# Performance work log

Hardware: AMD Instinct MI355X
Metric: run time of the kernel (lower is better)

The kernel has to match this reference:

```python
import jax, jax.numpy as jnp
import numpy as np

EPS = 1e-8  # torch.nn.CosineSimilarity default eps


def setup_inputs() -> dict:
    key = jax.random.key(0)
    batch = jax.random.normal(key, (8192, 128), dtype=jnp.float32)
    return {"batch": batch}


def reference(batch):
    B = batch.shape[0]
    # Full pairwise cosine similarity matrix S[i, j]
    norms = jnp.linalg.norm(batch, axis=1)                      # [B]
    denom = jnp.maximum(norms[:, None] * norms[None, :], EPS)   # [B, B]
    S = (batch @ batch.T) / denom                                # [B, B]
    # Denominator of soft_nll(i, j): sum_{m != i} exp(S[i, m])
    expS = jnp.exp(S)
    Z = expS.sum(axis=1) - jnp.diagonal(expS)                    # [B]
    logZ = jnp.log(Z)                                            # [B]
    # term(i, j) = -log( exp(S[i,j]) / Z_i ) = -S[i,j] + logZ_i
    # Original loop: for k in 1..(B+1)//2 - 1, pairs (2k-1, 2k) 1-indexed
    N = (B + 1) // 2
    ks = jnp.arange(1, N)
    i = 2 * ks - 2  # 0-indexed first element of pair
    j = 2 * ks - 1  # 0-indexed second element of pair
    pair_loss = (-S[i, j] + logZ[i]) + (-S[j, i] + logZ[j])
    return jnp.sum(pair_loss) / B
```

## Files before the change

### kernel.cpp

```cpp
#include <hip/hip_runtime.h>
#include <hip/hip_bf16.h>

typedef __attribute__((ext_vector_type(8))) short short8;
typedef __attribute__((ext_vector_type(4))) float floatx4;

#define B_ROWS 8192
#define DIM 128
#define NPAIR 4095
#define RSCALE 1.2011224087864498f

#define GLOAD_LDS16(gp, lp)                                                     \
    __builtin_amdgcn_global_load_lds(                                           \
        (const __attribute__((address_space(1))) void*)(gp),                    \
        (__attribute__((address_space(3))) void*)(lp), 16, 0, 0)

__global__ void kzero(float* __restrict__ Z) {
    int i = blockIdx.x * 256 + threadIdx.x;
    if (i < B_ROWS) Z[i] = 0.f;
}

__global__ void kprep(const float* __restrict__ X, __hip_bfloat16* __restrict__ XN,
                      float* __restrict__ pairT, float* __restrict__ out) {
    __shared__ float2 lds[4][64];
    const int wid = threadIdx.x >> 6;
    const int lane = threadIdx.x & 63;
    const int row = blockIdx.x * 4 + wid;

    const float2 v = *reinterpret_cast<const float2*>(X + row * DIM + lane * 2);
    float ss = v.x * v.x + v.y * v.y;
    #pragma unroll
    for (int m = 1; m < 64; m <<= 1) ss += __shfl_xor(ss, m, 64);
    const float rn = ss > 0.f ? rsqrtf(ss) : 0.f;
    const float2 nv = make_float2(v.x * rn, v.y * rn);

    *reinterpret_cast<__hip_bfloat162*>(XN + row * DIM + lane * 2) =
        __float22bfloat162_rn(make_float2(nv.x * RSCALE, nv.y * RSCALE));
    lds[wid][lane] = nv;
    __syncthreads();

    if ((wid & 1) == 0) {
        const int p = blockIdx.x * 2 + (wid >> 1);
        if (p < NPAIR) {
            const float2 a = lds[wid][lane];
            const float2 b = lds[wid + 1][lane];
            float d = a.x * b.x + a.y * b.y;
            #pragma unroll
            for (int m = 1; m < 64; m <<= 1) d += __shfl_xor(d, m, 64);
            if (lane == 0) pairT[p] = d;
        }
    }
    if (blockIdx.x == 0 && threadIdx.x == 0) out[0] = 0.f;
}

__device__ __forceinline__ void stage_half(const __hip_bfloat16* __restrict__ gsrc,
                                           __hip_bfloat16* lbuf, int tid) {
    const int wid = tid >> 6;
    const int lane = tid & 63;
    #pragma unroll
    for (int it = 0; it < 4; ++it) {
        const int woff = it * 2048 + wid * 512;
        const int e = woff + lane * 8;
        const int src = (e & ~127) | ((e & 127) ^ (((e >> 7) & 7) << 3));
        GLOAD_LDS16(gsrc + src, lbuf + woff);
    }
}

template <bool USEP>
__global__ void __launch_bounds__(256, 2) kgemm(const __hip_bfloat16* __restrict__ XN,
                                                float* __restrict__ ZP) {
    __shared__ __hip_bfloat16 Bs[3][64 * DIM];

    const int tid = threadIdx.x;
    const int wid = tid >> 6;
    const int lane = tid & 63;
    const int lr = lane & 15;
    const int lk = lane >> 4;
    const int wr = wid >> 1;
    const int wc = wid & 1;
    const int rb = blockIdx.y;
    const int g = blockIdx.x;

    short8 a[4][4];
    const __hip_bfloat16* Abase = XN + (rb * 128 + wr * 64 + lr) * DIM + lk * 8;
    #pragma unroll
    for (int m = 0; m < 4; ++m)
        #pragma unroll
        for (int kk = 0; kk < 4; ++kk)
            a[kk][m] = *reinterpret_cast<const short8*>(Abase + m * 16 * DIM + kk * 32);

    float rp[4][4];
    #pragma unroll
    for (int m = 0; m < 4; ++m)
        #pragma unroll
        for (int r = 0; r < 4; ++r) rp[m][r] = 0.f;

    const floatx4 zero4 = {0.f, 0.f, 0.f, 0.f};

    stage_half(XN + (size_t)(g * 8) * 128 * DIM, Bs[0], tid);
    stage_half(XN + ((size_t)(g * 8) * 128 + 64) * DIM, Bs[1], tid);

    for (int t = 0; t < 16; ++t) {
        if (t < 15)
            asm volatile("s_waitcnt vmcnt(4)" ::: "memory");
        else
            asm volatile("s_waitcnt vmcnt(0)" ::: "memory");
        __builtin_amdgcn_s_barrier();

        if (t + 2 < 16)
            stage_half(XN + ((size_t)(g * 8 + ((t + 2) >> 1)) * 128 + ((t + 2) & 1) * 64) * DIM,
                       Bs[(t + 2) % 3], tid);

        const __hip_bfloat16* Bt = Bs[t % 3];
        const int cbj = g * 8 + (t >> 1);
        const bool dzero = (cbj == rb) && ((t & 1) == wr);

        __builtin_amdgcn_s_setprio(1);
        short8 b[4][2];
        #pragma unroll
        for (int n = 0; n < 2; ++n) {
            const int row = wc * 32 + n * 16 + lr;
            #pragma unroll
            for (int kk = 0; kk < 4; ++kk) {
                const int col = (kk * 32 + lk * 8) ^ ((row & 7) << 3);
                b[kk][n] = *reinterpret_cast<const short8*>(&Bt[row * DIM + col]);
            }
        }

        floatx4 acc[4][2];
        #pragma unroll
        for (int m = 0; m < 4; ++m)
            #pragma unroll
            for (int n = 0; n < 2; ++n)
                acc[m][n] = __builtin_amdgcn_mfma_f32_16x16x32_bf16(a[0][m], b[0][n], zero4, 0, 0, 0);
        #pragma unroll
        for (int kk = 1; kk < 4; ++kk)
            #pragma unroll
            for (int m = 0; m < 4; ++m)
                #pragma unroll
                for (int n = 0; n < 2; ++n)
                    acc[m][n] = __builtin_amdgcn_mfma_f32_16x16x32_bf16(a[kk][m], b[kk][n], acc[m][n], 0, 0, 0);
        __builtin_amdgcn_s_setprio(0);

        if (dzero) {
            #pragma unroll
            for (int m = 0; m < 4; ++m)
                #pragma unroll
                for (int n = 0; n < 2; ++n)
                    #pragma unroll
                    for (int r = 0; r < 4; ++r) {
                        float e = __builtin_amdgcn_exp2f(acc[m][n][r]);
                        if (m * 16 + lk * 4 + r == wc * 32 + n * 16 + lr) e = 0.f;
                        rp[m][r] += e;
                    }
        } else {
            #pragma unroll
            for (int m = 0; m < 4; ++m)
                #pragma unroll
                for (int n = 0; n < 2; ++n)
                    #pragma unroll
                    for (int r = 0; r < 4; ++r)
                        rp[m][r] += __builtin_amdgcn_exp2f(acc[m][n][r]);
        }
    }

    #pragma unroll
    for (int m = 0; m < 4; ++m)
        #pragma unroll
        for (int r = 0; r < 4; ++r) {
            float v = rp[m][r];
            v += __shfl_xor(v, 1, 64);
            v += __shfl_xor(v, 2, 64);
            v += __shfl_xor(v, 4, 64);
            v += __shfl_xor(v, 8, 64);
            if (lr == 0) {
                const int row = rb * 128 + wr * 64 + m * 16 + lk * 4 + r;
                if (USEP)
                    ZP[(g * 2 + wc) * B_ROWS + row] = v;
                else
                    atomicAdd(&ZP[row], v);
            }
        }
}

__global__ void kfinalP(const float* __restrict__ P, const float* __restrict__ pairT,
                        float* __restrict__ out) {
    const int r = blockIdx.x * 256 + threadIdx.x;
    float s = 0.f;
    if (r < B_ROWS - 2) {
        float z = 0.f;
        #pragma unroll
        for (int tt = 0; tt < 16; ++tt) z += P[tt * B_ROWS + r];
        s = logf(z);
    }
    if (r < NPAIR) s -= 2.f * pairT[r];
    #pragma unroll
    for (int m = 1; m < 64; m <<= 1) s += __shfl_xor(s, m, 64);
    __shared__ float red[4];
    const int wid = threadIdx.x >> 6;
    const int lane = threadIdx.x & 63;
    if (lane == 0) red[wid] = s;
    __syncthreads();
    if (threadIdx.x == 0) {
        float tsum = red[0] + red[1] + red[2] + red[3];
        atomicAdd(out, tsum / (float)B_ROWS);
    }
}

__global__ void kfinalZ(const float* __restrict__ Z, const float* __restrict__ pairT,
                        float* __restrict__ out) {
    float s = 0.f;
    for (int r = threadIdx.x; r < B_ROWS - 2; r += 1024) s += logf(Z[r]);
    for (int p = threadIdx.x; p < NPAIR; p += 1024) s -= 2.f * pairT[p];
    #pragma unroll
    for (int m = 1; m < 64; m <<= 1) s += __shfl_xor(s, m, 64);
    __shared__ float red[16];
    const int wid = threadIdx.x >> 6;
    const int lane = threadIdx.x & 63;
    if (lane == 0) red[wid] = s;
    __syncthreads();
    if (threadIdx.x == 0) {
        float t = 0.f;
        #pragma unroll
        for (int i = 0; i < 16; ++i) t += red[i];
        out[0] = t / (float)B_ROWS;
    }
}

extern "C" void kernel_launch(void* const* d_in, const int* in_sizes, int n_in,
                              void* d_out, int out_size, void* d_ws, size_t ws_size,
                              hipStream_t stream) {
    (void)in_sizes; (void)n_in; (void)out_size;
    const float* X = (const float*)d_in[0];
    float* out = (float*)d_out;
    char* ws = (char*)d_ws;

    float* Z = (float*)ws;
    float* pairT = (float*)(ws + 32768);
    __hip_bfloat16* XN = (__hip_bfloat16*)(ws + 49152);
    float* P = (float*)(ws + 49152 + 2097152);
    const size_t need = 49152 + 2097152 + (size_t)16 * B_ROWS * 4;
    const bool useP = ws_size >= need;

    kprep<<<2048, 256, 0, stream>>>(X, XN, pairT, out);
    if (useP) {
        kgemm<true><<<dim3(8, 64), 256, 0, stream>>>(XN, P);
        kfinalP<<<32, 256, 0, stream>>>(P, pairT, out);
    } else {
        kzero<<<32, 256, 0, stream>>>(Z);
        kgemm<false><<<dim3(8, 64), 256, 0, stream>>>(XN, Z);
        kfinalZ<<<1, 1024, 0, stream>>>(Z, pairT, out);
    }
}
```

Measured before the change: 34.05 us.

## Exploit symmetry of the similarity matrix to halve GEMM and exp work

Each block now processes only block-diagonal offsets 0..32 of the 64x64 tile grid, scheduled as d = g + 11*i over an 11-wide grid. For off-diagonal tiles it accumulates exp row sums and also exp column sums, since exp(S) is symmetric. This roughly halves the MFMA and exp work. The cost is extra cross-lane shuffles and column-partial writes, and kfinalP must reduce 84 partial slots instead of 16, which raises workspace size and final-pass memory traffic.

```diff
diff --git a/kernel.cpp b/kernel.cpp
--- a/kernel.cpp
+++ b/kernel.cpp
@@ -7,6 +7,7 @@
 #define B_ROWS 8192
 #define DIM 128
 #define NPAIR 4095
+#define NSLOT 84
 #define RSCALE 1.2011224087864498f
 
 #define GLOAD_LDS16(gp, lp)                                                     \
@@ -96,23 +97,32 @@
 
     const floatx4 zero4 = {0.f, 0.f, 0.f, 0.f};
 
-    stage_half(XN + (size_t)(g * 8) * 128 * DIM, Bs[0], tid);
-    stage_half(XN + ((size_t)(g * 8) * 128 + 64) * DIM, Bs[1], tid);
-
-    for (int t = 0; t < 16; ++t) {
-        if (t < 15)
+    {
+        const size_t base = (size_t)(((rb + g) & 63) * 128) * DIM;
+        stage_half(XN + base, Bs[0], tid);
+        stage_half(XN + base + 64 * DIM, Bs[1], tid);
+    }
+
+    #pragma unroll
+    for (int s = 0; s < 6; ++s) {
+        if (s < 5)
             asm volatile("s_waitcnt vmcnt(4)" ::: "memory");
         else
             asm volatile("s_waitcnt vmcnt(0)" ::: "memory");
         __builtin_amdgcn_s_barrier();
 
-        if (t + 2 < 16)
-            stage_half(XN + ((size_t)(g * 8 + ((t + 2) >> 1)) * 128 + ((t + 2) & 1) * 64) * DIM,
-                       Bs[(t + 2) % 3], tid);
-
-        const __hip_bfloat16* Bt = Bs[t % 3];
-        const int cbj = g * 8 + (t >> 1);
-        const bool dzero = (cbj == rb) && ((t & 1) == wr);
+        if (s + 2 < 6) {
+            const int ii = (s + 2) >> 1, hh = (s + 2) & 1;
+            const int ccb = (rb + g + 11 * ii) & 63;
+            stage_half(XN + ((size_t)(ccb * 128) + hh * 64) * DIM, Bs[(s + 2) % 3], tid);
+        }
+
+        const int i = s >> 1, half = s & 1;
+        const int d = g + 11 * i;
+        const int cb = (rb + d) & 63;
+        const bool dzero = (d == 0) && (half == wr);
+        const bool docol = (d >= 1) && (d <= 31);
+        const __hip_bfloat16* Bt = Bs[s % 3];
 
         __builtin_amdgcn_s_setprio(1);
         short8 b[4][2];
@@ -141,25 +151,33 @@
                     acc[m][n] = __builtin_amdgcn_mfma_f32_16x16x32_bf16(a[kk][m], b[kk][n], acc[m][n], 0, 0, 0);
         __builtin_amdgcn_s_setprio(0);
 
-        if (dzero) {
-            #pragma unroll
-            for (int m = 0; m < 4; ++m)
+        float cp[2] = {0.f, 0.f};
+        #pragma unroll
+        for (int m = 0; m < 4; ++m)
+            #pragma unroll
+            for (int n = 0; n < 2; ++n)
                 #pragma unroll
-                for (int n = 0; n < 2; ++n)
-                    #pragma unroll
-                    for (int r = 0; r < 4; ++r) {
-                        float e = __builtin_amdgcn_exp2f(acc[m][n][r]);
-                        if (m * 16 + lk * 4 + r == wc * 32 + n * 16 + lr) e = 0.f;
-                        rp[m][r] += e;
-                    }
-        } else {
-            #pragma unroll
-            for (int m = 0; m < 4; ++m)
-                #pragma unroll
-                for (int n = 0; n < 2; ++n)
-                    #pragma unroll
-                    for (int r = 0; r < 4; ++r)
-                        rp[m][r] += __builtin_amdgcn_exp2f(acc[m][n][r]);
+                for (int r = 0; r < 4; ++r) {
+                    float e = __builtin_amdgcn_exp2f(acc[m][n][r]);
+                    if (dzero && (m * 16 + lk * 4 + r == wc * 32 + n * 16 + lr)) e = 0.f;
+                    rp[m][r] += e;
+                    cp[n] += e;
+                }
+
+        if (docol) {
+            #pragma unroll
+            for (int n = 0; n < 2; ++n) {
+                float v = cp[n];
+                v += __shfl_xor(v, 16, 64);
+                v += __shfl_xor(v, 32, 64);
+                if (lane < 16) {
+                    const int col = cb * 128 + half * 64 + wc * 32 + n * 16 + lr;
+                    if (USEP)
+                        ZP[(22 + (d - 1) * 2 + wr) * B_ROWS + col] = v;
+                    else
+                        atomicAdd(&ZP[col], v);
+                }
+            }
         }
     }
 
@@ -188,8 +206,7 @@
     float s = 0.f;
     if (r < B_ROWS - 2) {
         float z = 0.f;
-        #pragma unroll
-        for (int tt = 0; tt < 16; ++tt) z += P[tt * B_ROWS + r];
+        for (int tt = 0; tt < NSLOT; ++tt) z += P[tt * B_ROWS + r];
         s = logf(z);
     }
     if (r < NPAIR) s -= 2.f * pairT[r];
@@ -238,16 +255,16 @@
     float* pairT = (float*)(ws + 32768);
     __hip_bfloat16* XN = (__hip_bfloat16*)(ws + 49152);
     float* P = (float*)(ws + 49152 + 2097152);
-    const size_t need = 49152 + 2097152 + (size_t)16 * B_ROWS * 4;
+    const size_t need = 49152 + 2097152 + (size_t)NSLOT * B_ROWS * 4;
     const bool useP = ws_size >= need;
 
     kprep<<<2048, 256, 0, stream>>>(X, XN, pairT, out);
     if (useP) {
-        kgemm<true><<<dim3(8, 64), 256, 0, stream>>>(XN, P);
+        kgemm<true><<<dim3(11, 64), 256, 0, stream>>>(XN, P);
         kfinalP<<<32, 256, 0, stream>>>(P, pairT, out);
     } else {
         kzero<<<32, 256, 0, stream>>>(Z);
-        kgemm<false><<<dim3(8, 64), 256, 0, stream>>>(XN, Z);
+        kgemm<false><<<dim3(11, 64), 256, 0, stream>>>(XN, Z);
         kfinalZ<<<1, 1024, 0, stream>>>(Z, pairT, out);
     }
 }
```

Result: slower. 39.93 us (+17.3%).

## Fuse prep, GEMM and final reduction into one cooperative kernel with grid syncs

Applied to the files above, without the earlier changes.

Replaces the three-kernel chain (normalize, GEMM+exp row sums, final log reduction) with a single cooperative kernel that uses grid-wide syncs between phases. The aim is to remove launch gaps and inter-kernel overhead. The pair dot products are now read from the GEMM accumulators on diagonal tiles instead of being computed in the prep phase. This relies on all 512 blocks being co-resident, and the grid syncs add their own cost. If the cooperative launch fails, it falls back to the old path.

```diff
diff --git a/kernel.cpp b/kernel.cpp
--- a/kernel.cpp
+++ b/kernel.cpp
@@ -1,5 +1,8 @@
 #include <hip/hip_runtime.h>
 #include <hip/hip_bf16.h>
+#include <hip/hip_cooperative_groups.h>
+
+namespace cg = cooperative_groups;
 
 typedef __attribute__((ext_vector_type(8))) short short8;
 typedef __attribute__((ext_vector_type(4))) float floatx4;
@@ -8,15 +11,191 @@
 #define DIM 128
 #define NPAIR 4095
 #define RSCALE 1.2011224087864498f
+#define LN2F 0.6931471805599453f
 
 #define GLOAD_LDS16(gp, lp)                                                     \
     __builtin_amdgcn_global_load_lds(                                           \
         (const __attribute__((address_space(1))) void*)(gp),                    \
         (__attribute__((address_space(3))) void*)(lp), 16, 0, 0)
 
-__global__ void kzero(float* __restrict__ Z) {
-    int i = blockIdx.x * 256 + threadIdx.x;
-    if (i < B_ROWS) Z[i] = 0.f;
+__device__ __forceinline__ void stage_half(const __hip_bfloat16* __restrict__ gsrc,
+                                           __hip_bfloat16* lbuf, int tid) {
+    const int wid = tid >> 6;
+    const int lane = tid & 63;
+    #pragma unroll
+    for (int it = 0; it < 4; ++it) {
+        const int woff = it * 2048 + wid * 512;
+        const int e = woff + lane * 8;
+        const int src = (e & ~127) | ((e & 127) ^ (((e >> 7) & 7) << 3));
+        GLOAD_LDS16(gsrc + src, lbuf + woff);
+    }
+}
+
+__global__ void __launch_bounds__(256, 2) kfused(const float* __restrict__ X,
+                                                 __hip_bfloat16* __restrict__ XN,
+                                                 float* __restrict__ P,
+                                                 float* __restrict__ pairT,
+                                                 float* __restrict__ out) {
+    __shared__ __hip_bfloat16 Bs[3][64 * DIM];
+
+    const int tid = threadIdx.x;
+    const int wid = tid >> 6;
+    const int lane = tid & 63;
+    const int lr = lane & 15;
+    const int lk = lane >> 4;
+    const int wr = wid >> 1;
+    const int wc = wid & 1;
+    const int g = blockIdx.x;
+    const int rb = blockIdx.y;
+    const int bidl = rb * 8 + g;
+
+    #pragma unroll
+    for (int rr = 0; rr < 4; ++rr) {
+        const int row = bidl * 16 + wid * 4 + rr;
+        const float2 v = *reinterpret_cast<const float2*>(X + row * DIM + lane * 2);
+        float ss = v.x * v.x + v.y * v.y;
+        #pragma unroll
+        for (int m = 1; m < 64; m <<= 1) ss += __shfl_xor(ss, m, 64);
+        const float rn = (ss > 0.f ? rsqrtf(ss) : 0.f) * RSCALE;
+        *reinterpret_cast<__hip_bfloat162*>(XN + row * DIM + lane * 2) =
+            __float22bfloat162_rn(make_float2(v.x * rn, v.y * rn));
+    }
+    if (bidl == 0 && tid == 0) out[0] = 0.f;
+
+    cg::this_grid().sync();
+
+    {
+        short8 a[4][4];
+        const __hip_bfloat16* Abase = XN + (rb * 128 + wr * 64 + lr) * DIM + lk * 8;
+        #pragma unroll
+        for (int m = 0; m < 4; ++m)
+            #pragma unroll
+            for (int kk = 0; kk < 4; ++kk)
+                a[kk][m] = *reinterpret_cast<const short8*>(Abase + m * 16 * DIM + kk * 32);
+
+        float rp[4][4];
+        #pragma unroll
+        for (int m = 0; m < 4; ++m)
+            #pragma unroll
+            for (int r = 0; r < 4; ++r) rp[m][r] = 0.f;
+
+        const floatx4 zero4 = {0.f, 0.f, 0.f, 0.f};
+
+        stage_half(XN + (size_t)(g * 8) * 128 * DIM, Bs[0], tid);
+        stage_half(XN + ((size_t)(g * 8) * 128 + 64) * DIM, Bs[1], tid);
+
+        for (int t = 0; t < 16; ++t) {
+            if (t < 15)
+                asm volatile("s_waitcnt vmcnt(4)" ::: "memory");
+            else
+                asm volatile("s_waitcnt vmcnt(0)" ::: "memory");
+            __builtin_amdgcn_s_barrier();
+
+            if (t + 2 < 16)
+                stage_half(XN + ((size_t)(g * 8 + ((t + 2) >> 1)) * 128 + ((t + 2) & 1) * 64) * DIM,
+                           Bs[(t + 2) % 3], tid);
+
+            const __hip_bfloat16* Bt = Bs[t % 3];
+            const int cbj = g * 8 + (t >> 1);
+            const bool dzero = (cbj == rb) && ((t & 1) == wr);
+
+            __builtin_amdgcn_s_setprio(1);
+            short8 b[4][2];
+            #pragma unroll
+            for (int n = 0; n < 2; ++n) {
+                const int row = wc * 32 + n * 16 + lr;
+                #pragma unroll
+                for (int kk = 0; kk < 4; ++kk) {
+                    const int col = (kk * 32 + lk * 8) ^ ((row & 7) << 3);
+                    b[kk][n] = *reinterpret_cast<const short8*>(&Bt[row * DIM + col]);
+                }
+            }
+
+            floatx4 acc[4][2];
+            #pragma unroll
+            for (int m = 0; m < 4; ++m)
+                #pragma unroll
+                for (int n = 0; n < 2; ++n)
+                    acc[m][n] = __builtin_amdgcn_mfma_f32_16x16x32_bf16(a[0][m], b[0][n], zero4, 0, 0, 0);
+            #pragma unroll
+            for (int kk = 1; kk < 4; ++kk)
+                #pragma unroll
+                for (int m = 0; m < 4; ++m)
+                    #pragma unroll
+                    for (int n = 0; n < 2; ++n)
+                        acc[m][n] = __builtin_amdgcn_mfma_f32_16x16x32_bf16(a[kk][m], b[kk][n], acc[m][n], 0, 0, 0);
+            __builtin_amdgcn_s_setprio(0);
+
+            if (dzero) {
+                #pragma unroll
+                for (int m = 0; m < 4; ++m)
+                    #pragma unroll
+                    for (int n = 0; n < 2; ++n)
+                        #pragma unroll
+                        for (int r = 0; r < 4; ++r) {
+                            const int Rl = m * 16 + lk * 4 + r;
+                            const int Cl = wc * 32 + n * 16 + lr;
+                            const float av = acc[m][n][r];
+                            float e = __builtin_amdgcn_exp2f(av);
+                            if (Rl == Cl) e = 0.f;
+                            rp[m][r] += e;
+                            if (Cl == Rl + 1 && (Rl & 1) == 0) {
+                                const int Rg = rb * 128 + wr * 64 + Rl;
+                                if (Rg < B_ROWS - 2) pairT[Rg >> 1] = av * LN2F;
+                            }
+                        }
+            } else {
+                #pragma unroll
+                for (int m = 0; m < 4; ++m)
+                    #pragma unroll
+                    for (int n = 0; n < 2; ++n)
+                        #pragma unroll
+                        for (int r = 0; r < 4; ++r)
+                            rp[m][r] += __builtin_amdgcn_exp2f(acc[m][n][r]);
+            }
+        }
+
+        #pragma unroll
+        for (int m = 0; m < 4; ++m)
+            #pragma unroll
+            for (int r = 0; r < 4; ++r) {
+                float v = rp[m][r];
+                v += __shfl_xor(v, 1, 64);
+                v += __shfl_xor(v, 2, 64);
+                v += __shfl_xor(v, 4, 64);
+                v += __shfl_xor(v, 8, 64);
+                if (lr == 0) {
+                    const int row = rb * 128 + wr * 64 + m * 16 + lk * 4 + r;
+                    P[(g * 2 + wc) * B_ROWS + row] = v;
+                }
+            }
+    }
+
+    cg::this_grid().sync();
+
+    {
+        float s = 0.f;
+        if (tid < 16) {
+            const int r = bidl * 16 + tid;
+            if (r < B_ROWS - 2) {
+                float z = 0.f;
+                #pragma unroll
+                for (int t = 0; t < 16; ++t) z += P[t * B_ROWS + r];
+                s = logf(z);
+            }
+        } else if (tid < 24) {
+            const int p = bidl * 8 + (tid - 16);
+            if (p < NPAIR) s = -2.f * pairT[p];
+        }
+        #pragma unroll
+        for (int m = 1; m < 64; m <<= 1) s += __shfl_xor(s, m, 64);
+        float* red = (float*)&Bs[0][0];
+        __syncthreads();
+        if (lane == 0) red[wid] = s;
+        __syncthreads();
+        if (tid == 0)
+            atomicAdd(out, (red[0] + red[1] + red[2] + red[3]) / (float)B_ROWS);
+    }
 }
 
 __global__ void kprep(const float* __restrict__ X, __hip_bfloat16* __restrict__ XN,
@@ -52,20 +231,6 @@
     if (blockIdx.x == 0 && threadIdx.x == 0) out[0] = 0.f;
 }
 
-__device__ __forceinline__ void stage_half(const __hip_bfloat16* __restrict__ gsrc,
-                                           __hip_bfloat16* lbuf, int tid) {
-    const int wid = tid >> 6;
-    const int lane = tid & 63;
-    #pragma unroll
-    for (int it = 0; it < 4; ++it) {
-        const int woff = it * 2048 + wid * 512;
-        const int e = woff + lane * 8;
-        const int src = (e & ~127) | ((e & 127) ^ (((e >> 7) & 7) << 3));
-        GLOAD_LDS16(gsrc + src, lbuf + woff);
-    }
-}
-
-template <bool USEP>
 __global__ void __launch_bounds__(256, 2) kgemm(const __hip_bfloat16* __restrict__ XN,
                                                 float* __restrict__ ZP) {
     __shared__ __hip_bfloat16 Bs[3][64 * DIM];
@@ -174,10 +339,8 @@
             v += __shfl_xor(v, 8, 64);
             if (lr == 0) {
                 const int row = rb * 128 + wr * 64 + m * 16 + lk * 4 + r;
-                if (USEP)
-                    ZP[(g * 2 + wc) * B_ROWS + row] = v;
-                else
-                    atomicAdd(&ZP[row], v);
+                P_STORE:
+                ZP[(g * 2 + wc) * B_ROWS + row] = v;
             }
         }
 }
@@ -206,48 +369,24 @@
     }
 }
 
-__global__ void kfinalZ(const float* __restrict__ Z, const float* __restrict__ pairT,
-                        float* __restrict__ out) {
-    float s = 0.f;
-    for (int r = threadIdx.x; r < B_ROWS - 2; r += 1024) s += logf(Z[r]);
-    for (int p = threadIdx.x; p < NPAIR; p += 1024) s -= 2.f * pairT[p];
-    #pragma unroll
-    for (int m = 1; m < 64; m <<= 1) s += __shfl_xor(s, m, 64);
-    __shared__ float red[16];
-    const int wid = threadIdx.x >> 6;
-    const int lane = threadIdx.x & 63;
-    if (lane == 0) red[wid] = s;
-    __syncthreads();
-    if (threadIdx.x == 0) {
-        float t = 0.f;
-        #pragma unroll
-        for (int i = 0; i < 16; ++i) t += red[i];
-        out[0] = t / (float)B_ROWS;
-    }
-}
-
 extern "C" void kernel_launch(void* const* d_in, const int* in_sizes, int n_in,
                               void* d_out, int out_size, void* d_ws, size_t ws_size,
                               hipStream_t stream) {
-    (void)in_sizes; (void)n_in; (void)out_size;
+    (void)in_sizes; (void)n_in; (void)out_size; (void)ws_size;
     const float* X = (const float*)d_in[0];
     float* out = (float*)d_out;
     char* ws = (char*)d_ws;
 
-    float* Z = (float*)ws;
-    float* pairT = (float*)(ws + 32768);
-    __hip_bfloat16* XN = (__hip_bfloat16*)(ws + 49152);
-    float* P = (float*)(ws + 49152 + 2097152);
-    const size_t need = 49152 + 2097152 + (size_t)16 * B_ROWS * 4;
-    const bool useP = ws_size >= need;
-
-    kprep<<<2048, 256, 0, stream>>>(X, XN, pairT, out);
-    if (useP) {
-        kgemm<true><<<dim3(8, 64), 256, 0, stream>>>(XN, P);
+    float* pairT = (float*)ws;
+    __hip_bfloat16* XN = (__hip_bfloat16*)(ws + 32768);
+    float* P = (float*)(ws + 32768 + 2097152);
+
+    void* args[] = {(void*)&X, (void*)&XN, (void*)&P, (void*)&pairT, (void*)&out};
+    hipError_t e = hipLaunchCooperativeKernel((const void*)kfused, dim3(8, 64),
+                                              dim3(256), args, 0, stream);
+    if (e != hipSuccess) {
+        kprep<<<2048, 256, 0, stream>>>(X, XN, pairT, out);
+        kgemm<<<dim3(8, 64), 256, 0, stream>>>(XN, P);
         kfinalP<<<32, 256, 0, stream>>>(P, pairT, out);
-    } else {
-        kzero<<<32, 256, 0, stream>>>(Z);
-        kgemm<false><<<dim3(8, 64), 256, 0, stream>>>(XN, Z);
-        kfinalZ<<<1, 1024, 0, stream>>>(Z, pairT, out);
-    }
-}
+    }
+}
```

Measured after the change: 135.5 us. 3.98x slower.

## Switch Gram matrix to FP8 scaled MFMA 32x32x64 with doubled column split

Applied to the files above, without the earlier changes.

Normalized rows are now stored as FP8 (e4m3) instead of bf16, and the similarity GEMM uses the 32x32x64 scaled f8f6f4 MFMA. This halves the bytes for the operand and LDS tiles and doubles the math rate per instruction. The grid is split into 16 column groups (32 partial slots), so each block processes 8 tiles instead of 16. kprep now handles two rows per wave and computes the pair dot products with shuffles instead of LDS. FP8 quantization of the normalized vectors adds error in S and in the exponentiated sums, which may hurt the accuracy tolerance.

```diff
diff --git a/kernel.cpp b/kernel.cpp
--- a/kernel.cpp
+++ b/kernel.cpp
@@ -1,12 +1,14 @@
 #include <hip/hip_runtime.h>
 #include <hip/hip_bf16.h>
 
-typedef __attribute__((ext_vector_type(8))) short short8;
-typedef __attribute__((ext_vector_type(4))) float floatx4;
+typedef __attribute__((ext_vector_type(4))) int intx4;
+typedef __attribute__((ext_vector_type(8))) int intx8;
+typedef __attribute__((ext_vector_type(16))) float floatx16;
 
 #define B_ROWS 8192
 #define DIM 128
 #define NPAIR 4095
+#define NSLOT 32
 #define RSCALE 1.2011224087864498f
 
 #define GLOAD_LDS16(gp, lp)                                                     \
@@ -19,161 +21,159 @@
     if (i < B_ROWS) Z[i] = 0.f;
 }
 
-__global__ void kprep(const float* __restrict__ X, __hip_bfloat16* __restrict__ XN,
+__global__ void kprep(const float* __restrict__ X, unsigned char* __restrict__ XN,
                       float* __restrict__ pairT, float* __restrict__ out) {
-    __shared__ float2 lds[4][64];
     const int wid = threadIdx.x >> 6;
     const int lane = threadIdx.x & 63;
-    const int row = blockIdx.x * 4 + wid;
-
-    const float2 v = *reinterpret_cast<const float2*>(X + row * DIM + lane * 2);
-    float ss = v.x * v.x + v.y * v.y;
-    #pragma unroll
-    for (int m = 1; m < 64; m <<= 1) ss += __shfl_xor(ss, m, 64);
+    const int j = lane & 31;
+    const int W = blockIdx.x * 4 + wid;
+    const int row = 2 * W + (lane >> 5);
+
+    const float4 v = *reinterpret_cast<const float4*>(X + row * DIM + j * 4);
+    float ss = v.x * v.x + v.y * v.y + v.z * v.z + v.w * v.w;
+    #pragma unroll
+    for (int m = 1; m < 32; m <<= 1) ss += __shfl_xor(ss, m, 64);
     const float rn = ss > 0.f ? rsqrtf(ss) : 0.f;
-    const float2 nv = make_float2(v.x * rn, v.y * rn);
-
-    *reinterpret_cast<__hip_bfloat162*>(XN + row * DIM + lane * 2) =
-        __float22bfloat162_rn(make_float2(nv.x * RSCALE, nv.y * RSCALE));
-    lds[wid][lane] = nv;
-    __syncthreads();
-
-    if ((wid & 1) == 0) {
-        const int p = blockIdx.x * 2 + (wid >> 1);
-        if (p < NPAIR) {
-            const float2 a = lds[wid][lane];
-            const float2 b = lds[wid + 1][lane];
-            float d = a.x * b.x + a.y * b.y;
-            #pragma unroll
-            for (int m = 1; m < 64; m <<= 1) d += __shfl_xor(d, m, 64);
-            if (lane == 0) pairT[p] = d;
-        }
-    }
-    if (blockIdx.x == 0 && threadIdx.x == 0) out[0] = 0.f;
-}
-
-__device__ __forceinline__ void stage_half(const __hip_bfloat16* __restrict__ gsrc,
-                                           __hip_bfloat16* lbuf, int tid) {
-    const int wid = tid >> 6;
-    const int lane = tid & 63;
-    #pragma unroll
-    for (int it = 0; it < 4; ++it) {
-        const int woff = it * 2048 + wid * 512;
-        const int e = woff + lane * 8;
-        const int src = (e & ~127) | ((e & 127) ^ (((e >> 7) & 7) << 3));
-        GLOAD_LDS16(gsrc + src, lbuf + woff);
+
+    float4 pv;
+    pv.x = __shfl_xor(v.x, 32, 64);
+    pv.y = __shfl_xor(v.y, 32, 64);
+    pv.z = __shfl_xor(v.z, 32, 64);
+    pv.w = __shfl_xor(v.w, 32, 64);
+    float pd = v.x * pv.x + v.y * pv.y + v.z * pv.z + v.w * pv.w;
+    #pragma unroll
+    for (int m = 1; m < 32; m <<= 1) pd += __shfl_xor(pd, m, 64);
+    const float rno = __shfl_xor(rn, 32, 64);
+    if (lane == 0 && W < NPAIR) pairT[W] = pd * rn * rno;
+
+    const float sc = rn * RSCALE;
+    int pk = __builtin_amdgcn_cvt_pk_fp8_f32(v.x * sc, v.y * sc, 0, false);
+    pk = __builtin_amdgcn_cvt_pk_fp8_f32(v.z * sc, v.w * sc, pk, true);
+    reinterpret_cast<int*>(XN)[row * 32 + j] = pk;
+
+    if (W == 0 && lane == 0) out[0] = 0.f;
+}
+
+__device__ __forceinline__ void stage64(const unsigned char* __restrict__ gsrc,
+                                        unsigned char* lbuf, int tid) {
+    #pragma unroll
+    for (int it = 0; it < 2; ++it) {
+        const int off = it * 4096 + tid * 16;
+        const int src = (off & ~127) | ((off & 127) ^ (((off >> 7) & 7) << 4));
+        GLOAD_LDS16(gsrc + src, lbuf + off);
     }
 }
 
 template <bool USEP>
-__global__ void __launch_bounds__(256, 2) kgemm(const __hip_bfloat16* __restrict__ XN,
+__global__ void __launch_bounds__(256, 2) kgemm(const unsigned char* __restrict__ XN,
                                                 float* __restrict__ ZP) {
-    __shared__ __hip_bfloat16 Bs[3][64 * DIM];
+    __shared__ unsigned char Bs[3][64 * DIM];
 
     const int tid = threadIdx.x;
     const int wid = tid >> 6;
     const int lane = tid & 63;
-    const int lr = lane & 15;
-    const int lk = lane >> 4;
+    const int l31 = lane & 31;
+    const int hi = lane >> 5;
     const int wr = wid >> 1;
     const int wc = wid & 1;
     const int rb = blockIdx.y;
     const int g = blockIdx.x;
 
-    short8 a[4][4];
-    const __hip_bfloat16* Abase = XN + (rb * 128 + wr * 64 + lr) * DIM + lk * 8;
-    #pragma unroll
-    for (int m = 0; m < 4; ++m)
-        #pragma unroll
-        for (int kk = 0; kk < 4; ++kk)
-            a[kk][m] = *reinterpret_cast<const short8*>(Abase + m * 16 * DIM + kk * 32);
-
-    float rp[4][4];
-    #pragma unroll
-    for (int m = 0; m < 4; ++m)
-        #pragma unroll
-        for (int r = 0; r < 4; ++r) rp[m][r] = 0.f;
-
-    const floatx4 zero4 = {0.f, 0.f, 0.f, 0.f};
-
-    stage_half(XN + (size_t)(g * 8) * 128 * DIM, Bs[0], tid);
-    stage_half(XN + ((size_t)(g * 8) * 128 + 64) * DIM, Bs[1], tid);
-
-    for (int t = 0; t < 16; ++t) {
-        if (t < 15)
-            asm volatile("s_waitcnt vmcnt(4)" ::: "memory");
+    intx8 a[2][2];
+    #pragma unroll
+    for (int t = 0; t < 2; ++t) {
+        const unsigned char* Ab =
+            XN + (size_t)(rb * 128 + wr * 64 + t * 32 + l31) * DIM + hi * 32;
+        #pragma unroll
+        for (int kk = 0; kk < 2; ++kk)
+            a[kk][t] = *reinterpret_cast<const intx8*>(Ab + kk * 64);
+    }
+
+    float rp[2][16];
+    #pragma unroll
+    for (int t = 0; t < 2; ++t)
+        #pragma unroll
+        for (int q = 0; q < 16; ++q) rp[t][q] = 0.f;
+
+    const floatx16 z16 = {0.f, 0.f, 0.f, 0.f, 0.f, 0.f, 0.f, 0.f,
+                          0.f, 0.f, 0.f, 0.f, 0.f, 0.f, 0.f, 0.f};
+
+    stage64(XN + (size_t)(g * 512) * DIM, Bs[0], tid);
+    stage64(XN + (size_t)(g * 512 + 64) * DIM, Bs[1], tid);
+
+    const int rblk = (rb * 128 + wr * 64) >> 6;
+
+    for (int t = 0; t < 8; ++t) {
+        if (t < 7)
+            asm volatile("s_waitcnt vmcnt(2)" ::: "memory");
         else
             asm volatile("s_waitcnt vmcnt(0)" ::: "memory");
         __builtin_amdgcn_s_barrier();
 
-        if (t + 2 < 16)
-            stage_half(XN + ((size_t)(g * 8 + ((t + 2) >> 1)) * 128 + ((t + 2) & 1) * 64) * DIM,
-                       Bs[(t + 2) % 3], tid);
-
-        const __hip_bfloat16* Bt = Bs[t % 3];
-        const int cbj = g * 8 + (t >> 1);
-        const bool dzero = (cbj == rb) && ((t & 1) == wr);
+        if (t + 2 < 8)
+            stage64(XN + (size_t)(g * 512 + (t + 2) * 64) * DIM, Bs[(t + 2) % 3], tid);
+
+        const unsigned char* Bt = Bs[t % 3];
+        const int cbase = g * 512 + t * 64;
+        const int lcol = wc * 32 + l31;
 
         __builtin_amdgcn_s_setprio(1);
-        short8 b[4][2];
-        #pragma unroll
-        for (int n = 0; n < 2; ++n) {
-            const int row = wc * 32 + n * 16 + lr;
+        intx8 b[2];
+        #pragma unroll
+        for (int kk = 0; kk < 2; ++kk) {
+            const int base = kk * 64 + hi * 32;
+            const int sw = (lcol & 7) << 4;
+            const intx4 lo =
+                *reinterpret_cast<const intx4*>(&Bt[lcol * 128 + (base ^ sw)]);
+            const intx4 hi4 =
+                *reinterpret_cast<const intx4*>(&Bt[lcol * 128 + ((base + 16) ^ sw)]);
+            b[kk] = __builtin_shufflevector(lo, hi4, 0, 1, 2, 3, 4, 5, 6, 7);
+        }
+
+        floatx16 acc[2];
+        #pragma unroll
+        for (int tt = 0; tt < 2; ++tt) {
+            acc[tt] = __builtin_amdgcn_mfma_scale_f32_32x32x64_f8f6f4(
+                a[0][tt], b[0], z16, 0, 0, 0, 0x7F, 0, 0x7F);
+            acc[tt] = __builtin_amdgcn_mfma_scale_f32_32x32x64_f8f6f4(
+                a[1][tt], b[1], acc[tt], 0, 0, 0, 0x7F, 0, 0x7F);
+        }
+        __builtin_amdgcn_s_setprio(0);
+
+        if ((cbase >> 6) == rblk) {
+            const int ccol = cbase + wc * 32 + l31;
             #pragma unroll
-            for (int kk = 0; kk < 4; ++kk) {
-                const int col = (kk * 32 + lk * 8) ^ ((row & 7) << 3);
-                b[kk][n] = *reinterpret_cast<const short8*>(&Bt[row * DIM + col]);
-            }
-        }
-
-        floatx4 acc[4][2];
-        #pragma unroll
-        for (int m = 0; m < 4; ++m)
-            #pragma unroll
-            for (int n = 0; n < 2; ++n)
-                acc[m][n] = __builtin_amdgcn_mfma_f32_16x16x32_bf16(a[0][m], b[0][n], zero4, 0, 0, 0);
-        #pragma unroll
-        for (int kk = 1; kk < 4; ++kk)
-            #pragma unroll
-            for (int m = 0; m < 4; ++m)
+            for (int tt = 0; tt < 2; ++tt)
                 #pragma unroll
-                for (int n = 0; n < 2; ++n)
-                    acc[m][n] = __builtin_amdgcn_mfma_f32_16x16x32_bf16(a[kk][m], b[kk][n], acc[m][n], 0, 0, 0);
-        __builtin_amdgcn_s_setprio(0);
-
-        if (dzero) {
-            #pragma unroll
-            for (int m = 0; m < 4; ++m)
-                #pragma unroll
-                for (int n = 0; n < 2; ++n)
-                    #pragma unroll
-                    for (int r = 0; r < 4; ++r) {
-                        float e = __builtin_amdgcn_exp2f(acc[m][n][r]);
-                        if (m * 16 + lk * 4 + r == wc * 32 + n * 16 + lr) e = 0.f;
-                        rp[m][r] += e;
-                    }
+                for (int q = 0; q < 16; ++q) {
+                    const int rrow = rb * 128 + wr * 64 + tt * 32 +
+                                     (q & 3) + 8 * (q >> 2) + 4 * hi;
+                    float e = __builtin_amdgcn_exp2f(acc[tt][q]);
+                    if (rrow == ccol) e = 0.f;
+                    rp[tt][q] += e;
+                }
         } else {
             #pragma unroll
-            for (int m = 0; m < 4; ++m)
+            for (int tt = 0; tt < 2; ++tt)
                 #pragma unroll
-                for (int n = 0; n < 2; ++n)
-                    #pragma unroll
-                    for (int r = 0; r < 4; ++r)
-                        rp[m][r] += __builtin_amdgcn_exp2f(acc[m][n][r]);
-        }
-    }
-
-    #pragma unroll
-    for (int m = 0; m < 4; ++m)
-        #pragma unroll
-        for (int r = 0; r < 4; ++r) {
-            float v = rp[m][r];
+                for (int q = 0; q < 16; ++q)
+                    rp[tt][q] += __builtin_amdgcn_exp2f(acc[tt][q]);
+        }
+    }
+
+    #pragma unroll
+    for (int tt = 0; tt < 2; ++tt)
+        #pragma unroll
+        for (int q = 0; q < 16; ++q) {
+            float v = rp[tt][q];
             v += __shfl_xor(v, 1, 64);
             v += __shfl_xor(v, 2, 64);
             v += __shfl_xor(v, 4, 64);
             v += __shfl_xor(v, 8, 64);
-            if (lr == 0) {
-                const int row = rb * 128 + wr * 64 + m * 16 + lk * 4 + r;
+            v += __shfl_xor(v, 16, 64);
+            if (l31 == 0) {
+                const int row = rb * 128 + wr * 64 + tt * 32 +
+                                (q & 3) + 8 * (q >> 2) + 4 * hi;
                 if (USEP)
                     ZP[(g * 2 + wc) * B_ROWS + row] = v;
                 else
@@ -189,7 +189,7 @@
     if (r < B_ROWS - 2) {
         float z = 0.f;
         #pragma unroll
-        for (int tt = 0; tt < 16; ++tt) z += P[tt * B_ROWS + r];
+        for (int tt = 0; tt < NSLOT; ++tt) z += P[tt * B_ROWS + r];
         s = logf(z);
     }
     if (r < NPAIR) s -= 2.f * pairT[r];
@@ -236,18 +236,18 @@
 
     float* Z = (float*)ws;
     float* pairT = (float*)(ws + 32768);
-    __hip_bfloat16* XN = (__hip_bfloat16*)(ws + 49152);
-    float* P = (float*)(ws + 49152 + 2097152);
-    const size_t need = 49152 + 2097152 + (size_t)16 * B_ROWS * 4;
+    unsigned char* XN = (unsigned char*)(ws + 49152);
+    float* P = (float*)(ws + 49152 + 1048576);
+    const size_t need = 49152 + 1048576 + (size_t)NSLOT * B_ROWS * 4;
     const bool useP = ws_size >= need;
 
-    kprep<<<2048, 256, 0, stream>>>(X, XN, pairT, out);
+    kprep<<<1024, 256, 0, stream>>>(X, XN, pairT, out);
     if (useP) {
-        kgemm<true><<<dim3(8, 64), 256, 0, stream>>>(XN, P);
+        kgemm<true><<<dim3(16, 64), 256, 0, stream>>>(XN, P);
         kfinalP<<<32, 256, 0, stream>>>(P, pairT, out);
     } else {
         kzero<<<32, 256, 0, stream>>>(Z);
-        kgemm<false><<<dim3(8, 64), 256, 0, stream>>>(XN, Z);
+        kgemm<false><<<dim3(16, 64), 256, 0, stream>>>(XN, Z);
         kfinalZ<<<1, 1024, 0, stream>>>(Z, pairT, out);
     }
 }
```

New measurement: 65.29 us. 1.92x slower.
